# Kernel optimization log

Measured on AMD Instinct MI355X. Metric: run time of the kernel, lower is better.

Reference implementation:

```python
import jax, jax.numpy as jnp
import numpy as np
from math import sqrt

B, L, S = 8, 1024, 1000
D_MODEL, D_LLM, H, E = 1024, 4096, 16, 64  # d_keys = d_model // n_heads = 64


def setup_inputs() -> dict:
    key = jax.random.key(0)
    ks = jax.random.split(key, 11)
    s = 0.02
    return {
        "target_embedding": jax.random.normal(ks[0], (B, L, D_MODEL), jnp.float32),
        "source_embedding": jax.random.normal(ks[1], (S, D_LLM), jnp.float32),
        "value_embedding": jax.random.normal(ks[2], (S, D_LLM), jnp.float32),
        "Wq": jax.random.normal(ks[3], (D_MODEL, H * E), jnp.float32) * s,
        "bq": jnp.zeros((H * E,), jnp.float32),
        "Wk": jax.random.normal(ks[4], (D_LLM, H * E), jnp.float32) * s,
        "bk": jnp.zeros((H * E,), jnp.float32),
        "Wv": jax.random.normal(ks[5], (D_LLM, H * E), jnp.float32) * s,
        "bv": jnp.zeros((H * E,), jnp.float32),
        "Wo": jax.random.normal(ks[6], (H * E, D_LLM), jnp.float32) * s,
        "bo": jnp.zeros((D_LLM,), jnp.float32),
    }


def reference(target_embedding, source_embedding, value_embedding,
              Wq, bq, Wk, bk, Wv, bv, Wo, bo):
    b, l, _ = target_embedding.shape
    # projections
    q = (target_embedding @ Wq + bq).reshape(b, l, H, E)          # (B,L,H,E)
    k = (source_embedding @ Wk + bk).reshape(-1, H, E)            # (S,H,E) shared across batch
    v = (value_embedding @ Wv + bv).reshape(-1, H, E)             # (S,H,E)
    scale = 1.0 / sqrt(E)
    scores = jnp.einsum('blhe,she->bhls', q, k) * scale           # (B,H,L,S)
    A = jax.nn.softmax(scores, axis=-1)                           # dropout is identity (eval)
    out = jnp.einsum('bhls,she->blhe', A, v).reshape(b, l, H * E)
    return out @ Wo + bo                                          # (B,L,d_llm)
```

## Files before the change

### kernel.cpp

```cpp
#include <hip/hip_runtime.h>
#include <hip/hip_bf16.h>
#include <math.h>

#define B_SZ 8
#define L_SZ 1024
#define S_SZ 1000
#define DM   1024
#define DL   4096
#define NH   16
#define EH   64
#define QK_SCALE 0.180336880f

typedef __bf16 bf16x8 __attribute__((ext_vector_type(8)));
typedef __bf16 bf16x4 __attribute__((ext_vector_type(4)));
typedef float  f32x4  __attribute__((ext_vector_type(4)));

__device__ __forceinline__ void async16(const void* g, void* l) {
    __builtin_amdgcn_global_load_lds(
        (const __attribute__((address_space(1))) void*)g,
        (__attribute__((address_space(3))) void*)l, 16, 0, 0);
}

__global__ __launch_bounds__(256) void cast_all_kernel(
    const float* __restrict__ target, const float* __restrict__ source,
    const float* __restrict__ value, __bf16* __restrict__ Tb,
    __bf16* __restrict__ Sb, __bf16* __restrict__ Vb)
{
    int bid = blockIdx.x;
    const float* in; __bf16* out; int i;
    if (bid < 8192)       { in = target; out = Tb; i = bid * 256 + threadIdx.x; }
    else if (bid < 12192) { in = source; out = Sb; i = (bid - 8192)  * 256 + threadIdx.x; }
    else                  { in = value;  out = Vb; i = (bid - 12192) * 256 + threadIdx.x; }
    float4 x = ((const float4*)in)[i];
    bf16x4 y;
    y.x = (__bf16)x.x; y.y = (__bf16)x.y;
    y.z = (__bf16)x.z; y.w = (__bf16)x.w;
    ((bf16x4*)out)[i] = y;
}

__global__ __launch_bounds__(256) void transpose_all_kernel(
    const float* __restrict__ Wq, const float* __restrict__ Wk,
    const float* __restrict__ Wv, const float* __restrict__ Wo,
    __bf16* __restrict__ WqT, __bf16* __restrict__ WkT,
    __bf16* __restrict__ WvT, __bf16* __restrict__ WoT)
{
    __shared__ float t[64][68];
    int bid = blockIdx.x;
    const float* W; __bf16* WT; int K, N, bx, by;
    if (bid < 256)       { W = Wq; WT = WqT; K = DM; N = DM; int u = bid;        bx = u & 15; by = u >> 4; }
    else if (bid < 1280) { W = Wk; WT = WkT; K = DL; N = DM; int u = bid - 256;  bx = u & 15; by = u >> 4; }
    else if (bid < 2304) { W = Wv; WT = WvT; K = DL; N = DM; int u = bid - 1280; bx = u & 15; by = u >> 4; }
    else                 { W = Wo; WT = WoT; K = DM; N = DL; int u = bid - 2304; bx = u & 63; by = u >> 6; }
    const int k0 = by * 64, n0 = bx * 64;
    const int tx = threadIdx.x & 15, ty = threadIdx.x >> 4;

#pragma unroll
    for (int tt = 0; tt < 4; ++tt) {
        int r = ty + 16 * tt;
        float4 x = *(const float4*)&W[(size_t)(k0 + r) * N + n0 + 4 * tx];
        *(float4*)&t[r][4 * tx] = x;
    }
    __syncthreads();
#pragma unroll
    for (int tt = 0; tt < 4; ++tt) {
        int n = ty + 16 * tt;
        bf16x4 y;
        y.x = (__bf16)t[4 * tx + 0][n];
        y.y = (__bf16)t[4 * tx + 1][n];
        y.z = (__bf16)t[4 * tx + 2][n];
        y.w = (__bf16)t[4 * tx + 3][n];
        *(bf16x4*)&WT[(size_t)(n0 + n) * K + k0 + 4 * tx] = y;
    }
}

__global__ __launch_bounds__(256) void transpose_v_kernel(
    const __bf16* __restrict__ vb, __bf16* __restrict__ vtb)
{
    __shared__ __bf16 t[64][72];
    const int d0 = blockIdx.x * 64, s0 = blockIdx.y * 64;
    const int tid = threadIdx.x;
#pragma unroll
    for (int tt = 0; tt < 2; ++tt) {
        int idx = tt * 256 + tid;
        int r = idx >> 3, ch = idx & 7;
        bf16x8 val;
        if (s0 + r < S_SZ) {
            val = *(const bf16x8*)&vb[(size_t)(s0 + r) * DM + d0 + ch * 8];
        } else {
#pragma unroll
            for (int j = 0; j < 8; ++j) val[j] = (__bf16)0.f;
        }
        *(bf16x8*)&t[r][ch * 8] = val;
    }
    __syncthreads();
#pragma unroll
    for (int tt = 0; tt < 2; ++tt) {
        int idx = tt * 256 + tid;
        int r = idx >> 3, ch = idx & 7;
        bf16x8 o;
#pragma unroll
        for (int j = 0; j < 8; ++j) o[j] = t[ch * 8 + j][r];
        *(bf16x8*)&vtb[(size_t)(d0 + r) * 1024 + s0 + ch * 8] = o;
    }
}

template <bool OUT_BF16>
__device__ __forceinline__ void gemm_body(
    const __bf16* __restrict__ A, const __bf16* __restrict__ BT,
    const float* __restrict__ bias, void* __restrict__ Cv,
    int M, int N, int K, int bx, int by, float oscale,
    __bf16* As, __bf16* Bs)
{
    const int tid  = threadIdx.x;
    const int lane = tid & 63;
    const int wave = tid >> 6;
    const int wr   = wave >> 1;
    const int wc   = wave & 1;
    const int m0   = by * 128;
    const int n0   = bx * 128;
    const int lm   = lane & 15;
    const int lq   = lane >> 4;

    f32x4 acc[4][4];
#pragma unroll
    for (int i = 0; i < 4; ++i)
#pragma unroll
        for (int j = 0; j < 4; ++j)
            acc[i][j] = (f32x4){0.f, 0.f, 0.f, 0.f};

    for (int k0 = 0; k0 < K; k0 += 32) {
#pragma unroll
        for (int t = 0; t < 2; ++t) {
            int chunk = t * 256 + tid;
            int r     = chunk >> 2;
            int koff  = (chunk & 3) * 8;
            int gm = m0 + r; if (gm >= M) gm = M - 1;
            async16(A  + (size_t)gm * K + k0 + koff, (char*)As + chunk * 16);
            int gn = n0 + r;
            async16(BT + (size_t)gn * K + k0 + koff, (char*)Bs + chunk * 16);
        }
        __syncthreads();

        bf16x8 af[4], bf_[4];
#pragma unroll
        for (int i = 0; i < 4; ++i) {
            af[i]  = *(const bf16x8*)&As[(wr * 64 + i * 16 + lm) * 32 + lq * 8];
            bf_[i] = *(const bf16x8*)&Bs[(wc * 64 + i * 16 + lm) * 32 + lq * 8];
        }
#pragma unroll
        for (int i = 0; i < 4; ++i)
#pragma unroll
            for (int j = 0; j < 4; ++j)
                acc[i][j] = __builtin_amdgcn_mfma_f32_16x16x32_bf16(
                    af[i], bf_[j], acc[i][j], 0, 0, 0);
        __syncthreads();
    }

#pragma unroll
    for (int i = 0; i < 4; ++i) {
        int gm0 = m0 + wr * 64 + i * 16 + lq * 4;
#pragma unroll
        for (int j = 0; j < 4; ++j) {
            int gn = n0 + wc * 64 + j * 16 + lm;
            float bv = bias[gn];
#pragma unroll
            for (int r = 0; r < 4; ++r) {
                int gm = gm0 + r;
                if (gm < M) {
                    float val = (acc[i][j][r] + bv) * oscale;
                    if (OUT_BF16)
                        ((__bf16*)Cv)[(size_t)gm * N + gn] = (__bf16)val;
                    else
                        ((float*)Cv)[(size_t)gm * N + gn] = val;
                }
            }
        }
    }
}

template <bool OUT_BF16>
__global__ __launch_bounds__(256) void gemm_bt_kernel(
    const __bf16* __restrict__ A, const __bf16* __restrict__ BT,
    const float* __restrict__ bias, void* __restrict__ Cv,
    int M, int N, int K, float oscale)
{
    __shared__ __bf16 As[128 * 32];
    __shared__ __bf16 Bs[128 * 32];
    gemm_body<OUT_BF16>(A, BT, bias, Cv, M, N, K,
                        blockIdx.x, blockIdx.y, oscale, As, Bs);
}

__global__ __launch_bounds__(256) void qkv_fused_kernel(
    const __bf16* __restrict__ Tb, const __bf16* __restrict__ Sb,
    const __bf16* __restrict__ Vb,
    const __bf16* __restrict__ WqT, const __bf16* __restrict__ WkT,
    const __bf16* __restrict__ WvT,
    const float* __restrict__ bq, const float* __restrict__ bk,
    const float* __restrict__ bv,
    __bf16* __restrict__ qb, __bf16* __restrict__ kb, __bf16* __restrict__ vb)
{
    __shared__ __bf16 As[128 * 32];
    __shared__ __bf16 Bs[128 * 32];
    int bid = blockIdx.x;
    const __bf16 *A, *BT; const float* bias; __bf16* C;
    int M, K, bx, by; float osc;
    if (bid < 64)       { A = Sb; BT = WkT; bias = bk; C = kb; M = S_SZ; K = DL;
                          bx = bid & 7; by = bid >> 3; osc = 1.f; }
    else if (bid < 128) { int u = bid - 64;  A = Vb; BT = WvT; bias = bv; C = vb;
                          M = S_SZ; K = DL; bx = u & 7; by = u >> 3; osc = 1.f; }
    else                { int u = bid - 128; A = Tb; BT = WqT; bias = bq; C = qb;
                          M = B_SZ * L_SZ; K = DM; bx = u & 7; by = u >> 3; osc = QK_SCALE; }
    gemm_body<true>(A, BT, bias, C, M, DM, K, bx, by, osc, As, Bs);
}

__global__ __launch_bounds__(256) void attn_mfma_kernel(
    const __bf16* __restrict__ q,
    const __bf16* __restrict__ k,
    const __bf16* __restrict__ vt,
    __bf16* __restrict__ o)
{
    __shared__ __bf16 Ks [2][64 * 64];
    __shared__ __bf16 Vts[2][64 * 64];
    __shared__ __bf16 Ps [4][32 * 72];

    const int tid  = threadIdx.x;
    const int lane = tid & 63;
    const int wave = tid >> 6;
    const int lm   = lane & 15;
    const int lq   = lane >> 4;
    const int bh = blockIdx.y;
    const int b  = bh >> 4;
    const int h  = bh & 15;
    const int l0 = blockIdx.x * 128;
    const int row0 = b * L_SZ + l0 + wave * 32;

    bf16x8 qf[2][2];
#pragma unroll
    for (int mt = 0; mt < 2; ++mt)
#pragma unroll
        for (int ks = 0; ks < 2; ++ks)
            qf[mt][ks] = *(const bf16x8*)&q[(size_t)(row0 + mt * 16 + lm) * DM
                                           + h * 64 + ks * 32 + lq * 8];

    f32x4 oa[2][4];
    f32x4 lacc[2];
    float m_run[2][4];
#pragma unroll
    for (int mt = 0; mt < 2; ++mt) {
        lacc[mt] = (f32x4){0.f, 0.f, 0.f, 0.f};
#pragma unroll
        for (int r = 0; r < 4; ++r) m_run[mt][r] = -1e30f;
#pragma unroll
        for (int et = 0; et < 4; ++et) oa[mt][et] = (f32x4){0.f, 0.f, 0.f, 0.f};
    }

    bf16x8 vones;
#pragma unroll
    for (int j = 0; j < 8; ++j) vones[j] = (__bf16)1.0f;

    auto stage = [&](int bi, int s0v) {
#pragma unroll
        for (int t = 0; t < 2; ++t) {
            int cc = t * 256 + tid;
            int r = cc >> 3, segL = cc & 7;
            int segG = segL ^ (r & 7);
            int sg = s0v + r; if (sg >= S_SZ) sg = S_SZ - 1;
            async16(k  + (size_t)sg * DM + h * 64 + segG * 8,
                    (char*)Ks[bi] + cc * 16);
            async16(vt + (size_t)(h * 64 + r) * 1024 + s0v + segG * 8,
                    (char*)Vts[bi] + cc * 16);
        }
    };

    stage(0, 0);
    int cur = 0;

    for (int s0 = 0; s0 < S_SZ; s0 += 64) {
        __syncthreads();
        if (s0 + 64 < S_SZ) stage(cur ^ 1, s0 + 64);

        f32x4 sc[2][4];
#pragma unroll
        for (int mt = 0; mt < 2; ++mt)
#pragma unroll
            for (int nt = 0; nt < 4; ++nt)
                sc[mt][nt] = (f32x4){0.f, 0.f, 0.f, 0.f};
#pragma unroll
        for (int ks = 0; ks < 2; ++ks)
#pragma unroll
            for (int nt = 0; nt < 4; ++nt) {
                bf16x8 bK = *(const bf16x8*)((const char*)Ks[cur]
                    + (nt * 16 + lm) * 128 + (((ks * 4 + lq) ^ (lm & 7)) * 16));
#pragma unroll
                for (int mt = 0; mt < 2; ++mt)
                    sc[mt][nt] = __builtin_amdgcn_mfma_f32_16x16x32_bf16(
                        qf[mt][ks], bK, sc[mt][nt], 0, 0, 0);
            }

        if (s0 + 64 > S_SZ) {
#pragma unroll
            for (int nt = 0; nt < 4; ++nt) {
                bool masked = (s0 + nt * 16 + lm >= S_SZ);
                if (masked)
#pragma unroll
                    for (int mt = 0; mt < 2; ++mt)
#pragma unroll
                        for (int r = 0; r < 4; ++r) sc[mt][nt][r] = -1e30f;
            }
        }

        float pm[2][4];
        bool ok = true;
#pragma unroll
        for (int mt = 0; mt < 2; ++mt)
#pragma unroll
            for (int r = 0; r < 4; ++r) {
                pm[mt][r] = fmaxf(fmaxf(sc[mt][0][r], sc[mt][1][r]),
                                  fmaxf(sc[mt][2][r], sc[mt][3][r]));
                ok = ok && (pm[mt][r] <= m_run[mt][r] + 8.f);
            }
        if (!__all((int)ok)) {
#pragma unroll
            for (int mt = 0; mt < 2; ++mt)
#pragma unroll
                for (int r = 0; r < 4; ++r) {
                    float mx = pm[mt][r];
#pragma unroll
                    for (int off = 1; off < 16; off <<= 1)
                        mx = fmaxf(mx, __shfl_xor(mx, off));
                    float mnew  = fmaxf(m_run[mt][r], mx);
                    float alpha = __builtin_amdgcn_exp2f(m_run[mt][r] - mnew);
                    m_run[mt][r] = mnew;
                    lacc[mt][r] *= alpha;
#pragma unroll
                    for (int et = 0; et < 4; ++et)
                        oa[mt][et][r] *= alpha;
                }
        }

#pragma unroll
        for (int mt = 0; mt < 2; ++mt)
#pragma unroll
            for (int r = 0; r < 4; ++r) {
                int prow = (mt * 16 + lq * 4 + r) * 72;
#pragma unroll
                for (int nt = 0; nt < 4; ++nt) {
                    float pv = __builtin_amdgcn_exp2f(sc[mt][nt][r] - m_run[mt][r]);
                    Ps[wave][prow + nt * 16 + lm] = (__bf16)pv;
                }
            }

        asm volatile("s_waitcnt lgkmcnt(0)" ::: "memory");

#pragma unroll
        for (int ks = 0; ks < 2; ++ks) {
            bf16x8 aP[2];
#pragma unroll
            for (int mt = 0; mt < 2; ++mt)
                aP[mt] = *(const bf16x8*)&Ps[wave][(mt * 16 + lm) * 72
                                                  + ks * 32 + lq * 8];
#pragma unroll
            for (int mt = 0; mt < 2; ++mt)
                lacc[mt] = __builtin_amdgcn_mfma_f32_16x16x32_bf16(
                    aP[mt], vones, lacc[mt], 0, 0, 0);
#pragma unroll
            for (int et = 0; et < 4; ++et) {
                bf16x8 bV = *(const bf16x8*)((const char*)Vts[cur]
                    + (et * 16 + lm) * 128 + (((ks * 4 + lq) ^ (lm & 7)) * 16));
#pragma unroll
                for (int mt = 0; mt < 2; ++mt)
                    oa[mt][et] = __builtin_amdgcn_mfma_f32_16x16x32_bf16(
                        aP[mt], bV, oa[mt][et], 0, 0, 0);
            }
        }
        cur ^= 1;
    }

#pragma unroll
    for (int mt = 0; mt < 2; ++mt)
#pragma unroll
        for (int r = 0; r < 4; ++r) {
            float inv = 1.f / lacc[mt][r];
            size_t rowi = (size_t)(row0 + mt * 16 + lq * 4 + r) * DM + h * 64;
#pragma unroll
            for (int et = 0; et < 4; ++et)
                o[rowi + et * 16 + lm] = (__bf16)(oa[mt][et][r] * inv);
        }
}

extern "C" void kernel_launch(void* const* d_in, const int* in_sizes, int n_in,
                              void* d_out, int out_size, void* d_ws, size_t ws_size,
                              hipStream_t stream)
{
    const float* target = (const float*)d_in[0];
    const float* source = (const float*)d_in[1];
    const float* value  = (const float*)d_in[2];
    const float* Wq = (const float*)d_in[3];
    const float* bq = (const float*)d_in[4];
    const float* Wk = (const float*)d_in[5];
    const float* bk = (const float*)d_in[6];
    const float* Wv = (const float*)d_in[7];
    const float* bv = (const float*)d_in[8];
    const float* Wo = (const float*)d_in[9];
    const float* bo = (const float*)d_in[10];
    float* out = (float*)d_out;

    char* p = (char*)d_ws;
    __bf16* Tb  = (__bf16*)(p);
    __bf16* Sb  = (__bf16*)(p + 16777216);
    __bf16* vtb = (__bf16*)(p + 16777216);
    __bf16* kb  = (__bf16*)(p + 24969216);
    __bf16* vb  = (__bf16*)(p + 27017216);
    __bf16* WqT = (__bf16*)(p + 29065216);
    __bf16* WoT = (__bf16*)(p + 31162368);
    char*   R   =           p + 39550976;
    __bf16* Vb  = (__bf16*)(R);
    __bf16* WvT = (__bf16*)(R + 8192000);
    __bf16* WkT = (__bf16*)(R + 16580608);
    __bf16* qb  = (__bf16*)d_out;
    __bf16* ab  = (__bf16*)(p);

    const dim3 blk(256);

    cast_all_kernel<<<16192, blk, 0, stream>>>(target, source, value, Tb, Sb, Vb);
    transpose_all_kernel<<<3328, blk, 0, stream>>>(Wq, Wk, Wv, Wo, WqT, WkT, WvT, WoT);
    qkv_fused_kernel<<<640, blk, 0, stream>>>(Tb, Sb, Vb, WqT, WkT, WvT,
                                              bq, bk, bv, qb, kb, vb);
    transpose_v_kernel<<<dim3(16, 16), blk, 0, stream>>>(vb, vtb);
    attn_mfma_kernel<<<dim3(8, 128), blk, 0, stream>>>(qb, kb, vtb, ab);
    gemm_bt_kernel<false><<<dim3(32, 64), blk, 0, stream>>>(ab, WoT, bo, out,
                                                            B_SZ * L_SZ, DL, DM, 1.0f);
}
```

Measured before the change: 498.9 us.

## Split-K the K/V projections and use a pipelined 256x256 output GEMM

```diff
diff --git a/kernel.cpp b/kernel.cpp
--- a/kernel.cpp
+++ b/kernel.cpp
@@ -73,42 +73,12 @@
     }
 }
 
-__global__ __launch_bounds__(256) void transpose_v_kernel(
-    const __bf16* __restrict__ vb, __bf16* __restrict__ vtb)
-{
-    __shared__ __bf16 t[64][72];
-    const int d0 = blockIdx.x * 64, s0 = blockIdx.y * 64;
-    const int tid = threadIdx.x;
-#pragma unroll
-    for (int tt = 0; tt < 2; ++tt) {
-        int idx = tt * 256 + tid;
-        int r = idx >> 3, ch = idx & 7;
-        bf16x8 val;
-        if (s0 + r < S_SZ) {
-            val = *(const bf16x8*)&vb[(size_t)(s0 + r) * DM + d0 + ch * 8];
-        } else {
-#pragma unroll
-            for (int j = 0; j < 8; ++j) val[j] = (__bf16)0.f;
-        }
-        *(bf16x8*)&t[r][ch * 8] = val;
-    }
-    __syncthreads();
-#pragma unroll
-    for (int tt = 0; tt < 2; ++tt) {
-        int idx = tt * 256 + tid;
-        int r = idx >> 3, ch = idx & 7;
-        bf16x8 o;
-#pragma unroll
-        for (int j = 0; j < 8; ++j) o[j] = t[ch * 8 + j][r];
-        *(bf16x8*)&vtb[(size_t)(d0 + r) * 1024 + s0 + ch * 8] = o;
-    }
-}
-
-template <bool OUT_BF16>
+template <int OMODE>
 __device__ __forceinline__ void gemm_body(
-    const __bf16* __restrict__ A, const __bf16* __restrict__ BT,
+    const __bf16* __restrict__ A, int lda,
+    const __bf16* __restrict__ BT, int ldb,
     const float* __restrict__ bias, void* __restrict__ Cv,
-    int M, int N, int K, int bx, int by, float oscale,
+    int M, int N, int Kext, int bx, int by, float oscale,
     __bf16* As, __bf16* Bs)
 {
     const int tid  = threadIdx.x;
@@ -128,16 +98,16 @@
         for (int j = 0; j < 4; ++j)
             acc[i][j] = (f32x4){0.f, 0.f, 0.f, 0.f};
 
-    for (int k0 = 0; k0 < K; k0 += 32) {
+    for (int k0 = 0; k0 < Kext; k0 += 32) {
 #pragma unroll
         for (int t = 0; t < 2; ++t) {
             int chunk = t * 256 + tid;
             int r     = chunk >> 2;
             int koff  = (chunk & 3) * 8;
             int gm = m0 + r; if (gm >= M) gm = M - 1;
-            async16(A  + (size_t)gm * K + k0 + koff, (char*)As + chunk * 16);
+            async16(A  + (size_t)gm * lda + k0 + koff, (char*)As + chunk * 16);
             int gn = n0 + r;
-            async16(BT + (size_t)gn * K + k0 + koff, (char*)Bs + chunk * 16);
+            async16(BT + (size_t)gn * ldb + k0 + koff, (char*)Bs + chunk * 16);
         }
         __syncthreads();
 
@@ -162,32 +132,20 @@
 #pragma unroll
         for (int j = 0; j < 4; ++j) {
             int gn = n0 + wc * 64 + j * 16 + lm;
-            float bv = bias[gn];
+            float bv = (OMODE == 0) ? bias[gn] : 0.f;
 #pragma unroll
             for (int r = 0; r < 4; ++r) {
                 int gm = gm0 + r;
                 if (gm < M) {
-                    float val = (acc[i][j][r] + bv) * oscale;
-                    if (OUT_BF16)
-                        ((__bf16*)Cv)[(size_t)gm * N + gn] = (__bf16)val;
+                    if (OMODE == 0)
+                        ((__bf16*)Cv)[(size_t)gm * N + gn] =
+                            (__bf16)((acc[i][j][r] + bv) * oscale);
                     else
-                        ((float*)Cv)[(size_t)gm * N + gn] = val;
+                        ((float*)Cv)[(size_t)gm * N + gn] = acc[i][j][r];
                 }
             }
         }
     }
-}
-
-template <bool OUT_BF16>
-__global__ __launch_bounds__(256) void gemm_bt_kernel(
-    const __bf16* __restrict__ A, const __bf16* __restrict__ BT,
-    const float* __restrict__ bias, void* __restrict__ Cv,
-    int M, int N, int K, float oscale)
-{
-    __shared__ __bf16 As[128 * 32];
-    __shared__ __bf16 Bs[128 * 32];
-    gemm_body<OUT_BF16>(A, BT, bias, Cv, M, N, K,
-                        blockIdx.x, blockIdx.y, oscale, As, Bs);
 }
 
 __global__ __launch_bounds__(256) void qkv_fused_kernel(
@@ -195,22 +153,192 @@
     const __bf16* __restrict__ Vb,
     const __bf16* __restrict__ WqT, const __bf16* __restrict__ WkT,
     const __bf16* __restrict__ WvT,
-    const float* __restrict__ bq, const float* __restrict__ bk,
-    const float* __restrict__ bv,
-    __bf16* __restrict__ qb, __bf16* __restrict__ kb, __bf16* __restrict__ vb)
+    const float* __restrict__ bq,
+    __bf16* __restrict__ qb, float* __restrict__ kpart, float* __restrict__ vpart)
 {
     __shared__ __bf16 As[128 * 32];
     __shared__ __bf16 Bs[128 * 32];
     int bid = blockIdx.x;
-    const __bf16 *A, *BT; const float* bias; __bf16* C;
-    int M, K, bx, by; float osc;
-    if (bid < 64)       { A = Sb; BT = WkT; bias = bk; C = kb; M = S_SZ; K = DL;
-                          bx = bid & 7; by = bid >> 3; osc = 1.f; }
-    else if (bid < 128) { int u = bid - 64;  A = Vb; BT = WvT; bias = bv; C = vb;
-                          M = S_SZ; K = DL; bx = u & 7; by = u >> 3; osc = 1.f; }
-    else                { int u = bid - 128; A = Tb; BT = WqT; bias = bq; C = qb;
-                          M = B_SZ * L_SZ; K = DM; bx = u & 7; by = u >> 3; osc = QK_SCALE; }
-    gemm_body<true>(A, BT, bias, C, M, DM, K, bx, by, osc, As, Bs);
+    if (bid < 512) {
+        int proj = bid >> 8;
+        int u  = bid & 255;
+        int ks = u >> 6;
+        int v  = u & 63;
+        const __bf16* Aop = (proj ? Vb : Sb) + ks * 1024;
+        const __bf16* Bop = (proj ? WvT : WkT) + ks * 1024;
+        float* Cp = (proj ? vpart : kpart) + (size_t)ks * 1024000;
+        gemm_body<2>(Aop, DL, Bop, DL, nullptr, Cp, S_SZ, DM, 1024,
+                     v & 7, v >> 3, 1.f, As, Bs);
+    } else {
+        int u = bid - 512;
+        gemm_body<0>(Tb, DM, WqT, DM, bq, qb, B_SZ * L_SZ, DM, DM,
+                     u & 7, u >> 3, QK_SCALE, As, Bs);
+    }
+}
+
+__global__ __launch_bounds__(256) void combine_kv_kernel(
+    const float* __restrict__ kpart, const float* __restrict__ vpart,
+    const float* __restrict__ bk, const float* __restrict__ bv,
+    __bf16* __restrict__ kb, __bf16* __restrict__ vtb)
+{
+    __shared__ float t[64][68];
+    const int bid = blockIdx.x, tid = threadIdx.x;
+    if (bid < 1000) {
+        int e4 = bid * 256 + tid;
+        int col = (e4 & 255) * 4;
+        float4 s = *(const float4*)&bk[col];
+#pragma unroll
+        for (int j = 0; j < 4; ++j) {
+            float4 pp = *(const float4*)&kpart[(size_t)j * 1024000 + (size_t)e4 * 4];
+            s.x += pp.x; s.y += pp.y; s.z += pp.z; s.w += pp.w;
+        }
+        bf16x4 y;
+        y.x = (__bf16)s.x; y.y = (__bf16)s.y;
+        y.z = (__bf16)s.z; y.w = (__bf16)s.w;
+        ((bf16x4*)kb)[e4] = y;
+    } else {
+        int u = bid - 1000;
+        int d0 = (u & 15) * 64, s0 = (u >> 4) * 64;
+#pragma unroll
+        for (int tt = 0; tt < 4; ++tt) {
+            int idx = tt * 256 + tid;
+            int r = idx >> 4, c4 = idx & 15;
+            float4 s = {0.f, 0.f, 0.f, 0.f};
+            if (s0 + r < S_SZ) {
+                s = *(const float4*)&bv[d0 + c4 * 4];
+#pragma unroll
+                for (int j = 0; j < 4; ++j) {
+                    float4 pp = *(const float4*)&vpart[(size_t)j * 1024000
+                                + (size_t)(s0 + r) * 1024 + d0 + c4 * 4];
+                    s.x += pp.x; s.y += pp.y; s.z += pp.z; s.w += pp.w;
+                }
+            }
+            *(float4*)&t[r][c4 * 4] = s;
+        }
+        __syncthreads();
+#pragma unroll
+        for (int tt = 0; tt < 2; ++tt) {
+            int idx = tt * 256 + tid;
+            int d = idx >> 3, ch = idx & 7;
+            bf16x8 o;
+#pragma unroll
+            for (int j = 0; j < 8; ++j) o[j] = (__bf16)t[ch * 8 + j][d];
+            *(bf16x8*)&vtb[(size_t)(d0 + d) * 1024 + s0 + ch * 8] = o;
+        }
+    }
+}
+
+__global__ __launch_bounds__(512, 2) void gemm_o8_kernel(
+    const __bf16* __restrict__ A, const __bf16* __restrict__ BT,
+    const float* __restrict__ bias, float* __restrict__ C)
+{
+    __shared__ __bf16 sA[3][256 * 32];
+    __shared__ __bf16 sB[3][256 * 32];
+    const int tid  = threadIdx.x;
+    const int lane = tid & 63, wave = tid >> 6;
+    const int wr = wave >> 2, wc = wave & 3;
+    const int lm = lane & 15, lq = lane >> 4;
+    const int K = 1024, NT = 32;
+
+    int bid = blockIdx.x;
+    bid = (bid & 7) * 64 + (bid >> 3);
+    const int bx = bid & 15, by = bid >> 4;
+    const int m0 = by * 256, n0 = bx * 256;
+
+    f32x4 acc[8][4];
+#pragma unroll
+    for (int i = 0; i < 8; ++i)
+#pragma unroll
+        for (int j = 0; j < 4; ++j)
+            acc[i][j] = (f32x4){0.f, 0.f, 0.f, 0.f};
+
+    auto stage = [&](int slot, int t) {
+        const int k0 = t * 32;
+#pragma unroll
+        for (int i = 0; i < 2; ++i) {
+            int cc = i * 512 + tid;
+            int r  = cc >> 2;
+            int sg = (cc & 3) ^ ((r >> 1) & 3);
+            async16(A  + (size_t)(m0 + r) * K + k0 + sg * 8,
+                    (char*)sA[slot] + cc * 16);
+            async16(BT + (size_t)(n0 + r) * K + k0 + sg * 8,
+                    (char*)sB[slot] + cc * 16);
+        }
+    };
+
+    stage(0, 0);
+    stage(1, 1);
+    asm volatile("s_waitcnt vmcnt(4)" ::: "memory");
+    __builtin_amdgcn_s_barrier();
+    __builtin_amdgcn_sched_barrier(0);
+
+    int sl = 0;
+    for (int t = 0; t < NT; ++t) {
+        if (t + 2 < NT) {
+            int s2 = sl + 2; if (s2 >= 3) s2 -= 3;
+            stage(s2, t + 2);
+        }
+        bf16x8 fb[4], fa[8];
+#pragma unroll
+        for (int ni = 0; ni < 4; ++ni) {
+            int rr = wc * 64 + ni * 16 + lm;
+            fb[ni] = *(const bf16x8*)((const char*)sB[sl]
+                     + rr * 64 + ((lq ^ ((rr >> 1) & 3)) * 16));
+        }
+#pragma unroll
+        for (int mi = 0; mi < 4; ++mi) {
+            int rr = wr * 128 + mi * 16 + lm;
+            fa[mi] = *(const bf16x8*)((const char*)sA[sl]
+                     + rr * 64 + ((lq ^ ((rr >> 1) & 3)) * 16));
+        }
+        __builtin_amdgcn_sched_barrier(0);
+#pragma unroll
+        for (int mi = 4; mi < 8; ++mi) {
+            int rr = wr * 128 + mi * 16 + lm;
+            fa[mi] = *(const bf16x8*)((const char*)sA[sl]
+                     + rr * 64 + ((lq ^ ((rr >> 1) & 3)) * 16));
+        }
+        asm volatile("s_waitcnt lgkmcnt(4)" ::: "memory");
+        __builtin_amdgcn_sched_barrier(0);
+        __builtin_amdgcn_s_setprio(1);
+#pragma unroll
+        for (int mi = 0; mi < 4; ++mi)
+#pragma unroll
+            for (int ni = 0; ni < 4; ++ni)
+                acc[mi][ni] = __builtin_amdgcn_mfma_f32_16x16x32_bf16(
+                    fa[mi], fb[ni], acc[mi][ni], 0, 0, 0);
+        __builtin_amdgcn_s_setprio(0);
+        asm volatile("s_waitcnt lgkmcnt(0)" ::: "memory");
+        __builtin_amdgcn_sched_barrier(0);
+        __builtin_amdgcn_s_setprio(1);
+#pragma unroll
+        for (int mi = 4; mi < 8; ++mi)
+#pragma unroll
+            for (int ni = 0; ni < 4; ++ni)
+                acc[mi][ni] = __builtin_amdgcn_mfma_f32_16x16x32_bf16(
+                    fa[mi], fb[ni], acc[mi][ni], 0, 0, 0);
+        __builtin_amdgcn_s_setprio(0);
+        if (t + 2 < NT)
+            asm volatile("s_waitcnt vmcnt(4)" ::: "memory");
+        else
+            asm volatile("s_waitcnt vmcnt(0)" ::: "memory");
+        __builtin_amdgcn_s_barrier();
+        __builtin_amdgcn_sched_barrier(0);
+        if (++sl == 3) sl = 0;
+    }
+
+#pragma unroll
+    for (int mi = 0; mi < 8; ++mi) {
+        int gm0 = m0 + wr * 128 + mi * 16 + lq * 4;
+#pragma unroll
+        for (int ni = 0; ni < 4; ++ni) {
+            int gn = n0 + wc * 64 + ni * 16 + lm;
+            float bv = bias[gn];
+#pragma unroll
+            for (int r = 0; r < 4; ++r)
+                C[(size_t)(gm0 + r) * 4096 + gn] = acc[mi][ni][r] + bv;
+        }
+    }
 }
 
 __global__ __launch_bounds__(256) void attn_mfma_kernel(
@@ -410,24 +538,24 @@
     __bf16* Sb  = (__bf16*)(p + 16777216);
     __bf16* vtb = (__bf16*)(p + 16777216);
     __bf16* kb  = (__bf16*)(p + 24969216);
-    __bf16* vb  = (__bf16*)(p + 27017216);
     __bf16* WqT = (__bf16*)(p + 29065216);
     __bf16* WoT = (__bf16*)(p + 31162368);
     char*   R   =           p + 39550976;
     __bf16* Vb  = (__bf16*)(R);
     __bf16* WvT = (__bf16*)(R + 8192000);
     __bf16* WkT = (__bf16*)(R + 16580608);
-    __bf16* qb  = (__bf16*)d_out;
-    __bf16* ab  = (__bf16*)(p);
+    __bf16* qb    = (__bf16*)d_out;
+    float*  kpart = (float*)((char*)d_out + 16777216);
+    float*  vpart = (float*)((char*)d_out + 33161216);
+    __bf16* ab    = (__bf16*)(p);
 
     const dim3 blk(256);
 
     cast_all_kernel<<<16192, blk, 0, stream>>>(target, source, value, Tb, Sb, Vb);
     transpose_all_kernel<<<3328, blk, 0, stream>>>(Wq, Wk, Wv, Wo, WqT, WkT, WvT, WoT);
-    qkv_fused_kernel<<<640, blk, 0, stream>>>(Tb, Sb, Vb, WqT, WkT, WvT,
-                                              bq, bk, bv, qb, kb, vb);
-    transpose_v_kernel<<<dim3(16, 16), blk, 0, stream>>>(vb, vtb);
+    qkv_fused_kernel<<<1024, blk, 0, stream>>>(Tb, Sb, Vb, WqT, WkT, WvT,
+                                               bq, qb, kpart, vpart);
+    combine_kv_kernel<<<1256, blk, 0, stream>>>(kpart, vpart, bk, bv, kb, vtb);
     attn_mfma_kernel<<<dim3(8, 128), blk, 0, stream>>>(qb, kb, vtb, ab);
-    gemm_bt_kernel<false><<<dim3(32, 64), blk, 0, stream>>>(ab, WoT, bo, out,
-                                                            B_SZ * L_SZ, DL, DM, 1.0f);
-}
+    gemm_o8_kernel<<<512, 512, 0, stream>>>(ab, WoT, bo, out);
+}
```

Result: faster. 451.6 us (-9.5%).
